# Optimization experiments

Measured on AMD Instinct MI355X. Metric: run time of the kernel, lower is better.

The kernel has to match this reference:

```python
import jax, jax.numpy as jnp
import numpy as np

# lower-triangular (row, col) positions in packed order: (0,0),(1,0),(1,1),(2,0),(2,1),(2,2)
_ROWS = np.array([0, 1, 1, 2, 2, 2])
_COLS = np.array([0, 0, 1, 0, 1, 2])


def setup_inputs() -> dict:
    key = jax.random.key(0)
    chol_cov = jax.random.normal(key, (8388608, 6), dtype=jnp.float32)
    return {"chol_cov": chol_cov}


def reference(chol_cov):
    bn = chol_cov.shape[0]
    # scatter packed vector into lower-triangular L: [bn, 3, 3]
    L = jnp.zeros((bn, 3, 3), dtype=chol_cov.dtype).at[:, _ROWS, _COLS].set(chol_cov)
    # Q = L @ L^T, batched 3x3 matmul
    Q = jnp.einsum('bij,bkj->bik', L, L)
    return Q
```

## Files before the change

### kernel.cpp

```cpp
#include <hip/hip_runtime.h>


__global__ __launch_bounds__(256) void getcov_kernel(
    const float* __restrict__ in, float* __restrict__ out, int npairs) {
    int t = blockIdx.x * blockDim.x + threadIdx.x;
    if (t >= npairs) return;

    const float4* __restrict__ in4 = reinterpret_cast<const float4*>(in + (size_t)t * 12);
    float4 v0 = in4[0];
    float4 v1 = in4[1];
    float4 v2 = in4[2];

    float a0 = v0.x, b0 = v0.y, c0 = v0.z, d0 = v0.w, e0 = v1.x, f0 = v1.y;
    float a1 = v1.z, b1 = v1.w, c1 = v2.x, d1 = v2.y, e1 = v2.z, f1 = v2.w;

    float q0_00 = a0 * a0;
    float q0_01 = a0 * b0;
    float q0_02 = a0 * d0;
    float q0_11 = b0 * b0 + c0 * c0;
    float q0_12 = b0 * d0 + c0 * e0;
    float q0_22 = d0 * d0 + e0 * e0 + f0 * f0;

    float q1_00 = a1 * a1;
    float q1_01 = a1 * b1;
    float q1_02 = a1 * d1;
    float q1_11 = b1 * b1 + c1 * c1;
    float q1_12 = b1 * d1 + c1 * e1;
    float q1_22 = d1 * d1 + e1 * e1 + f1 * f1;

    float2* __restrict__ o2 = reinterpret_cast<float2*>(out + (size_t)t * 18);
    o2[0] = make_float2(q0_00, q0_01);
    o2[1] = make_float2(q0_02, q0_01);
    o2[2] = make_float2(q0_11, q0_12);
    o2[3] = make_float2(q0_02, q0_12);
    o2[4] = make_float2(q0_22, q1_00);
    o2[5] = make_float2(q1_01, q1_02);
    o2[6] = make_float2(q1_01, q1_11);
    o2[7] = make_float2(q1_12, q1_02);
    o2[8] = make_float2(q1_12, q1_22);
}

extern "C" void kernel_launch(void* const* d_in, const int* in_sizes, int n_in,
                              void* d_out, int out_size, void* d_ws, size_t ws_size,
                              hipStream_t stream) {
    const float* in = (const float*)d_in[0];
    float* out = (float*)d_out;
    int n = in_sizes[0] / 6;
    int npairs = n / 2;
    int block = 256;
    int grid = (npairs + block - 1) / block;
    getcov_kernel<<<grid, block, 0, stream>>>(in, out, npairs);
}
```

Measured before the change: 466.8 us.

## Stage input and output through LDS for fully coalesced float4 global accesses

Each block now loads 1024 packed matrices into shared memory with contiguous float4 reads, computes in registers, writes the 3x3 results back into LDS, and stores them to global memory with contiguous float4 writes. This removes the strided per-thread 48-byte loads and 72-byte float2 stores of the old version, so every global access is fully coalesced. The cost is three barriers per block, LDS bank conflicts from the stride-6 and stride-9 accesses, and 36 KB of LDS per block, which limits occupancy. The grid now assumes the batch size is a multiple of 1024 and has no tail handling.

```diff
diff --git a/kernel.cpp b/kernel.cpp
--- a/kernel.cpp
+++ b/kernel.cpp
@@ -1,53 +1,64 @@
 #include <hip/hip_runtime.h>
 
 
-__global__ __launch_bounds__(256) void getcov_kernel(
-    const float* __restrict__ in, float* __restrict__ out, int npairs) {
-    int t = blockIdx.x * blockDim.x + threadIdx.x;
-    if (t >= npairs) return;
+constexpr int B = 1024;
+constexpr int T = 256;
 
-    const float4* __restrict__ in4 = reinterpret_cast<const float4*>(in + (size_t)t * 12);
-    float4 v0 = in4[0];
-    float4 v1 = in4[1];
-    float4 v2 = in4[2];
+__global__ __launch_bounds__(T) void getcov_kernel(
+    const float* __restrict__ in, float* __restrict__ out) {
+  __shared__ float4 lds4[(9 * B) / 4];
+  float* lds = reinterpret_cast<float*>(lds4);
 
-    float a0 = v0.x, b0 = v0.y, c0 = v0.z, d0 = v0.w, e0 = v1.x, f0 = v1.y;
-    float a1 = v1.z, b1 = v1.w, c1 = v2.x, d1 = v2.y, e1 = v2.z, f1 = v2.w;
+  const int tid = threadIdx.x;
+  const size_t base_b = (size_t)blockIdx.x * B;
 
-    float q0_00 = a0 * a0;
-    float q0_01 = a0 * b0;
-    float q0_02 = a0 * d0;
-    float q0_11 = b0 * b0 + c0 * c0;
-    float q0_12 = b0 * d0 + c0 * e0;
-    float q0_22 = d0 * d0 + e0 * e0 + f0 * f0;
+  const float4* __restrict__ gin =
+      reinterpret_cast<const float4*>(in) + (base_b * 6) / 4;
+#pragma unroll
+  for (int j = 0; j < 6; ++j) {
+    lds4[tid + T * j] = gin[tid + T * j];
+  }
+  __syncthreads();
 
-    float q1_00 = a1 * a1;
-    float q1_01 = a1 * b1;
-    float q1_02 = a1 * d1;
-    float q1_11 = b1 * b1 + c1 * c1;
-    float q1_12 = b1 * d1 + c1 * e1;
-    float q1_22 = d1 * d1 + e1 * e1 + f1 * f1;
+  float q[4][6];
+#pragma unroll
+  for (int j = 0; j < 4; ++j) {
+    const int b = tid + T * j;
+    const float* p = &lds[6 * b];
+    const float a = p[0], bb = p[1], c = p[2], d = p[3], e = p[4], f = p[5];
+    q[j][0] = a * a;
+    q[j][1] = a * bb;
+    q[j][2] = a * d;
+    q[j][3] = bb * bb + c * c;
+    q[j][4] = bb * d + c * e;
+    q[j][5] = d * d + e * e + f * f;
+  }
+  __syncthreads();
 
-    float2* __restrict__ o2 = reinterpret_cast<float2*>(out + (size_t)t * 18);
-    o2[0] = make_float2(q0_00, q0_01);
-    o2[1] = make_float2(q0_02, q0_01);
-    o2[2] = make_float2(q0_11, q0_12);
-    o2[3] = make_float2(q0_02, q0_12);
-    o2[4] = make_float2(q0_22, q1_00);
-    o2[5] = make_float2(q1_01, q1_02);
-    o2[6] = make_float2(q1_01, q1_11);
-    o2[7] = make_float2(q1_12, q1_02);
-    o2[8] = make_float2(q1_12, q1_22);
+#pragma unroll
+  for (int j = 0; j < 4; ++j) {
+    const int b = tid + T * j;
+    float* o = &lds[9 * b];
+    o[0] = q[j][0]; o[1] = q[j][1]; o[2] = q[j][2];
+    o[3] = q[j][1]; o[4] = q[j][3]; o[5] = q[j][4];
+    o[6] = q[j][2]; o[7] = q[j][4]; o[8] = q[j][5];
+  }
+  __syncthreads();
+
+  float4* __restrict__ gout =
+      reinterpret_cast<float4*>(out) + (base_b * 9) / 4;
+#pragma unroll
+  for (int j = 0; j < 9; ++j) {
+    gout[tid + T * j] = lds4[tid + T * j];
+  }
 }
 
 extern "C" void kernel_launch(void* const* d_in, const int* in_sizes, int n_in,
                               void* d_out, int out_size, void* d_ws, size_t ws_size,
                               hipStream_t stream) {
-    const float* in = (const float*)d_in[0];
-    float* out = (float*)d_out;
-    int n = in_sizes[0] / 6;
-    int npairs = n / 2;
-    int block = 256;
-    int grid = (npairs + block - 1) / block;
-    getcov_kernel<<<grid, block, 0, stream>>>(in, out, npairs);
+  const float* in = (const float*)d_in[0];
+  float* out = (float*)d_out;
+  const int nbatch = in_sizes[0] / 6;
+  const int grid = nbatch / B;
+  getcov_kernel<<<grid, T, 0, stream>>>(in, out);
 }
```

Measured after the change: 422.9 us. 1.1x faster.
